# Kernel optimization log

Hardware: AMD Instinct MI355X
Metric: run time of the kernel (lower is better)

The kernel has to match this reference:

```python
import jax, jax.numpy as jnp
import numpy as np


def _l2_normalize(x):
    # matches features.div(features.norm(2, 1, keepdim=True))
    return x / jnp.linalg.norm(x, ord=2, axis=1, keepdims=True)


def setup_inputs() -> dict:
    key = jax.random.key(0)
    k1, k2, k3 = jax.random.split(key, 3)
    B, N, D, C = 2048, 100000, 512, 1000
    return {
        "features": jax.random.normal(k1, (B, D), dtype=jnp.float32),
        "logits": jax.random.normal(k2, (B, C), dtype=jnp.float32),
        "db_features": jax.random.normal(k3, (N, D), dtype=jnp.float32),
        "k": 10,
    }


def reference(features, logits, db_features, k):
    # fit(): index.add(normalize(db_features)) -- faiss IndexFlatL2 stores rows
    xb = _l2_normalize(db_features)            # [N, D]
    # forward(): search normalized queries, take k-th (largest of the k) squared L2 dist
    xq = _l2_normalize(features)               # [B, D]
    # squared L2 distances via the expansion ||q||^2 + ||x||^2 - 2 q.x (faiss IndexFlatL2
    # returns SQUARED distances)
    q2 = jnp.sum(xq * xq, axis=1, keepdims=True)           # [B, 1]
    x2 = jnp.sum(xb * xb, axis=1)                          # [N]
    d2 = q2 + x2[None, :] - 2.0 * (xq @ xb.T)              # [B, N]
    # k smallest distances == k largest of -d2
    neg_topk, _ = jax.lax.top_k(-d2, k)                    # [B, k], sorted descending
    kth = -neg_topk[:, -1]                                 # k-th nearest squared distance
    return kth.reshape(-1, 1)
```

## Files before the change

### kernel.cpp

```cpp
#include <hip/hip_runtime.h>
#include <hip/hip_bf16.h>

typedef unsigned short ushort_t;
typedef unsigned char uchar_t;
typedef __attribute__((ext_vector_type(4))) int int4v;
typedef __attribute__((ext_vector_type(2))) unsigned int uint2v;

#define NQ      2048
#define ND      512
#define NDB     100000
#define TOPK    10
#define NCHUNK  98
#define CHUNK_N 1024
#define NPAD    (NCHUNK * CHUNK_N)
#define QTILES  (NQ / 128)
#define NTILES  (CHUNK_N / 128)
#define NWG     (NCHUNK * QTILES)
#define PERXCD  (NWG / 8)
#define QSCALE  400.0f
#define QINV    (1.0f / (QSCALE * QSCALE))
#define IMIN    (-2147483647 - 1)

#define GL2LDS(gp, lp) __builtin_amdgcn_global_load_lds(                      \
    (const __attribute__((address_space(1))) void*)(gp),                     \
    (__attribute__((address_space(3))) void*)(lp), 16, 0, 0)

__global__ void normalize_rows_i8(const float* __restrict__ in, uchar_t* __restrict__ out,
                                  int nvalid, int ntotal) {
    int row  = blockIdx.x * 4 + (threadIdx.x >> 6);
    int lane = threadIdx.x & 63;
    if (row >= ntotal) return;
    uint2v pk;
    if (row >= nvalid) {
        pk[0] = 0u; pk[1] = 0u;
    } else {
        const float4* src = reinterpret_cast<const float4*>(in + (size_t)row * ND);
        float4 v0 = src[lane * 2];
        float4 v1 = src[lane * 2 + 1];
        float s = v0.x*v0.x + v0.y*v0.y + v0.z*v0.z + v0.w*v0.w
                + v1.x*v1.x + v1.y*v1.y + v1.z*v1.z + v1.w*v1.w;
        #pragma unroll
        for (int off = 32; off; off >>= 1) s += __shfl_xor(s, off, 64);
        float r = rsqrtf(s) * QSCALE;
        float f[8] = { v0.x, v0.y, v0.z, v0.w, v1.x, v1.y, v1.z, v1.w };
        unsigned b[8];
        #pragma unroll
        for (int i = 0; i < 8; ++i) {
            int q = (int)rintf(f[i] * r);
            q = q > 127 ? 127 : (q < -127 ? -127 : q);
            b[i] = (unsigned)q & 0xFFu;
        }
        pk[0] = b[0] | (b[1] << 8) | (b[2] << 16) | (b[3] << 24);
        pk[1] = b[4] | (b[5] << 8) | (b[6] << 16) | (b[7] << 24);
    }
    *reinterpret_cast<uint2v*>(out + (size_t)row * ND + lane * 8) = pk;
}

__device__ inline void topk_insert_i(int (&top)[TOPK], int x) {
    #pragma unroll
    for (int i = 0; i < TOPK; ++i) {
        int mx = top[i] > x ? top[i] : x;
        int mn = top[i] > x ? x : top[i];
        top[i] = mx;
        x = mn;
    }
}

__global__ __launch_bounds__(512, 8)
void knn_chunk(const uchar_t* __restrict__ qb, const uchar_t* __restrict__ dbb,
               int* __restrict__ partial) {
    const int logical = (blockIdx.x & 7) * PERXCD + (blockIdx.x >> 3);
    const int qt = logical & (QTILES - 1);
    const int nc = logical >> 4;
    const int t = threadIdx.x, lane = t & 63, wv = t >> 6;
    const int l15 = lane & 15;

    __shared__ __align__(16) uchar_t As[128 * 64];
    __shared__ __align__(16) uchar_t Bs[128 * 64];

    int top[TOPK];
    #pragma unroll
    for (int i = 0; i < TOPK; ++i) top[i] = IMIN;

    const size_t nchunkbase = (size_t)nc * CHUNK_N;
    const uchar_t* aseg = qb + (size_t)(qt * 128) * ND;

    const int srow = t >> 2;
    const int scol = (t & 3) ^ ((srow >> 1) & 3);
    const int soff = srow * ND + scol * 16;
    const int doff = t * 16;
    const int cgrp = lane >> 4;
    const int slot = (cgrp ^ ((l15 >> 1) & 3)) * 16;
    const int aoff = (wv * 16 + l15) * 64 + slot;
    const int boff = l15 * 64 + slot;

    for (int nt = 0; nt < NTILES; ++nt) {
        const uchar_t* bseg = dbb + (nchunkbase + nt * 128) * ND;
        int4v acc[8];
        #pragma unroll
        for (int b = 0; b < 8; ++b) acc[b] = (int4v){0, 0, 0, 0};

        #pragma unroll
        for (int ks = 0; ks < 8; ++ks) {
            const int kbase = ks * 64;
            __syncthreads();
            GL2LDS(aseg + soff + kbase, As + doff);
            GL2LDS(bseg + soff + kbase, Bs + doff);
            __syncthreads();
            int4v af = *reinterpret_cast<const int4v*>(As + aoff);
            {
                int4v bf0 = *reinterpret_cast<const int4v*>(Bs + boff);
                int4v bf1 = *reinterpret_cast<const int4v*>(Bs + boff + 1024);
                int4v bf2 = *reinterpret_cast<const int4v*>(Bs + boff + 2048);
                int4v bf3 = *reinterpret_cast<const int4v*>(Bs + boff + 3072);
                acc[0] = __builtin_amdgcn_mfma_i32_16x16x64_i8(bf0, af, acc[0], 0, 0, 0);
                acc[1] = __builtin_amdgcn_mfma_i32_16x16x64_i8(bf1, af, acc[1], 0, 0, 0);
                acc[2] = __builtin_amdgcn_mfma_i32_16x16x64_i8(bf2, af, acc[2], 0, 0, 0);
                acc[3] = __builtin_amdgcn_mfma_i32_16x16x64_i8(bf3, af, acc[3], 0, 0, 0);
            }
            {
                int4v bf4 = *reinterpret_cast<const int4v*>(Bs + boff + 4096);
                int4v bf5 = *reinterpret_cast<const int4v*>(Bs + boff + 5120);
                int4v bf6 = *reinterpret_cast<const int4v*>(Bs + boff + 6144);
                int4v bf7 = *reinterpret_cast<const int4v*>(Bs + boff + 7168);
                acc[4] = __builtin_amdgcn_mfma_i32_16x16x64_i8(bf4, af, acc[4], 0, 0, 0);
                acc[5] = __builtin_amdgcn_mfma_i32_16x16x64_i8(bf5, af, acc[5], 0, 0, 0);
                acc[6] = __builtin_amdgcn_mfma_i32_16x16x64_i8(bf6, af, acc[6], 0, 0, 0);
                acc[7] = __builtin_amdgcn_mfma_i32_16x16x64_i8(bf7, af, acc[7], 0, 0, 0);
            }
        }

        int m = acc[0][0];
        #pragma unroll
        for (int ns = 0; ns < 8; ++ns)
            #pragma unroll
            for (int r = 0; r < 4; ++r)
                m = m > acc[ns][r] ? m : acc[ns][r];
        if (m > top[TOPK - 1]) {
            #pragma unroll
            for (int ns = 0; ns < 8; ++ns)
                #pragma unroll
                for (int r = 0; r < 4; ++r) {
                    int v = acc[ns][r];
                    if (v > top[TOPK - 1]) topk_insert_i(top, v);
                }
        }
    }

    #pragma unroll
    for (int step = 16; step <= 32; step <<= 1) {
        int other[TOPK];
        #pragma unroll
        for (int i = 0; i < TOPK; ++i) other[i] = __shfl_xor(top[i], step, 64);
        #pragma unroll
        for (int i = 0; i < TOPK; ++i)
            if (other[i] > top[TOPK - 1]) topk_insert_i(top, other[i]);
    }

    if ((lane >> 4) == 0) {
        const int q = qt * 128 + wv * 16 + l15;
        int* dst = partial + ((size_t)nc * NQ + q) * TOPK;
        #pragma unroll
        for (int i = 0; i < TOPK; ++i) dst[i] = top[i];
    }
}

__global__ void final_merge(const int* __restrict__ partial, float* __restrict__ out) {
    const int q = blockIdx.x * 4 + (threadIdx.x >> 6);
    const int lane = threadIdx.x & 63;
    if (q >= NQ) return;
    int top[TOPK];
    #pragma unroll
    for (int i = 0; i < TOPK; ++i) top[i] = IMIN;
    for (int c = lane; c < NCHUNK; c += 64) {
        const int* p = partial + ((size_t)c * NQ + q) * TOPK;
        #pragma unroll
        for (int i = 0; i < TOPK; ++i) {
            int x = p[i];
            if (x > top[TOPK - 1]) topk_insert_i(top, x);
        }
    }
    #pragma unroll
    for (int step = 1; step <= 32; step <<= 1) {
        int other[TOPK];
        #pragma unroll
        for (int i = 0; i < TOPK; ++i) other[i] = __shfl_xor(top[i], step, 64);
        #pragma unroll
        for (int i = 0; i < TOPK; ++i)
            if (other[i] > top[TOPK - 1]) topk_insert_i(top, other[i]);
    }
    if (lane == 0) out[q] = 2.0f - 2.0f * ((float)top[TOPK - 1] * QINV);
}

extern "C" void kernel_launch(void* const* d_in, const int* in_sizes, int n_in,
                              void* d_out, int out_size, void* d_ws, size_t ws_size,
                              hipStream_t stream) {
    const float* features = (const float*)d_in[0];
    const float* dbf      = (const float*)d_in[2];
    float* out = (float*)d_out;

    uchar_t* dbb = (uchar_t*)d_ws;
    uchar_t* qbn = dbb + (size_t)NPAD * ND;
    int* partial = (int*)(qbn + (size_t)NQ * ND);

    normalize_rows_i8<<<NPAD / 4, 256, 0, stream>>>(dbf, dbb, NDB, NPAD);
    normalize_rows_i8<<<NQ / 4, 256, 0, stream>>>(features, qbn, NQ, NQ);
    knn_chunk<<<NWG, 512, 0, stream>>>(qbn, dbb, partial);
    final_merge<<<NQ / 4, 256, 0, stream>>>(partial, out);
}
```

Measured before the change: 301.6 us.

## Double-buffer LDS tiles to overlap global-to-LDS loads with MFMA

```diff
diff --git a/kernel.cpp b/kernel.cpp
--- a/kernel.cpp
+++ b/kernel.cpp
@@ -75,8 +75,8 @@
     const int t = threadIdx.x, lane = t & 63, wv = t >> 6;
     const int l15 = lane & 15;
 
-    __shared__ __align__(16) uchar_t As[128 * 64];
-    __shared__ __align__(16) uchar_t Bs[128 * 64];
+    __shared__ __align__(16) uchar_t As[2][128 * 64];
+    __shared__ __align__(16) uchar_t Bs[2][128 * 64];
 
     int top[TOPK];
     #pragma unroll
@@ -94,6 +94,12 @@
     const int aoff = (wv * 16 + l15) * 64 + slot;
     const int boff = l15 * 64 + slot;
 
+    {
+        const uchar_t* bseg0 = dbb + nchunkbase * ND;
+        GL2LDS(aseg + soff, As[0] + doff);
+        GL2LDS(bseg0 + soff, Bs[0] + doff);
+    }
+
     for (int nt = 0; nt < NTILES; ++nt) {
         const uchar_t* bseg = dbb + (nchunkbase + nt * 128) * ND;
         int4v acc[8];
@@ -102,27 +108,36 @@
 
         #pragma unroll
         for (int ks = 0; ks < 8; ++ks) {
-            const int kbase = ks * 64;
-            __syncthreads();
-            GL2LDS(aseg + soff + kbase, As + doff);
-            GL2LDS(bseg + soff + kbase, Bs + doff);
-            __syncthreads();
-            int4v af = *reinterpret_cast<const int4v*>(As + aoff);
+            asm volatile("s_waitcnt vmcnt(0)" ::: "memory");
+            __builtin_amdgcn_s_barrier();
+            asm volatile("" ::: "memory");
+
+            if (ks < 7) {
+                GL2LDS(aseg + soff + (ks + 1) * 64, As[(ks + 1) & 1] + doff);
+                GL2LDS(bseg + soff + (ks + 1) * 64, Bs[(ks + 1) & 1] + doff);
+            } else if (nt + 1 < NTILES) {
+                GL2LDS(aseg + soff, As[0] + doff);
+                GL2LDS(bseg + 128 * ND + soff, Bs[0] + doff);
+            }
+
+            const uchar_t* Ac = As[ks & 1];
+            const uchar_t* Bc = Bs[ks & 1];
+            int4v af = *reinterpret_cast<const int4v*>(Ac + aoff);
             {
-                int4v bf0 = *reinterpret_cast<const int4v*>(Bs + boff);
-                int4v bf1 = *reinterpret_cast<const int4v*>(Bs + boff + 1024);
-                int4v bf2 = *reinterpret_cast<const int4v*>(Bs + boff + 2048);
-                int4v bf3 = *reinterpret_cast<const int4v*>(Bs + boff + 3072);
+                int4v bf0 = *reinterpret_cast<const int4v*>(Bc + boff);
+                int4v bf1 = *reinterpret_cast<const int4v*>(Bc + boff + 1024);
+                int4v bf2 = *reinterpret_cast<const int4v*>(Bc + boff + 2048);
+                int4v bf3 = *reinterpret_cast<const int4v*>(Bc + boff + 3072);
                 acc[0] = __builtin_amdgcn_mfma_i32_16x16x64_i8(bf0, af, acc[0], 0, 0, 0);
                 acc[1] = __builtin_amdgcn_mfma_i32_16x16x64_i8(bf1, af, acc[1], 0, 0, 0);
                 acc[2] = __builtin_amdgcn_mfma_i32_16x16x64_i8(bf2, af, acc[2], 0, 0, 0);
                 acc[3] = __builtin_amdgcn_mfma_i32_16x16x64_i8(bf3, af, acc[3], 0, 0, 0);
             }
             {
-                int4v bf4 = *reinterpret_cast<const int4v*>(Bs + boff + 4096);
-                int4v bf5 = *reinterpret_cast<const int4v*>(Bs + boff + 5120);
-                int4v bf6 = *reinterpret_cast<const int4v*>(Bs + boff + 6144);
-                int4v bf7 = *reinterpret_cast<const int4v*>(Bs + boff + 7168);
+                int4v bf4 = *reinterpret_cast<const int4v*>(Bc + boff + 4096);
+                int4v bf5 = *reinterpret_cast<const int4v*>(Bc + boff + 5120);
+                int4v bf6 = *reinterpret_cast<const int4v*>(Bc + boff + 6144);
+                int4v bf7 = *reinterpret_cast<const int4v*>(Bc + boff + 7168);
                 acc[4] = __builtin_amdgcn_mfma_i32_16x16x64_i8(bf4, af, acc[4], 0, 0, 0);
                 acc[5] = __builtin_amdgcn_mfma_i32_16x16x64_i8(bf5, af, acc[5], 0, 0, 0);
                 acc[6] = __builtin_amdgcn_mfma_i32_16x16x64_i8(bf6, af, acc[6], 0, 0, 0);
```

New measurement: 344.7 us. 14.3% more time.

## Retile wave work to 32 queries by 64 db rows per wave

Applied to the files above, without the earlier changes.

```diff
diff --git a/kernel.cpp b/kernel.cpp
--- a/kernel.cpp
+++ b/kernel.cpp
@@ -74,13 +74,16 @@
     const int nc = logical >> 4;
     const int t = threadIdx.x, lane = t & 63, wv = t >> 6;
     const int l15 = lane & 15;
+    const int qg = wv >> 1, nh = wv & 1;
 
     __shared__ __align__(16) uchar_t As[128 * 64];
     __shared__ __align__(16) uchar_t Bs[128 * 64];
 
-    int top[TOPK];
-    #pragma unroll
-    for (int i = 0; i < TOPK; ++i) top[i] = IMIN;
+    int top[2][TOPK];
+    #pragma unroll
+    for (int qs = 0; qs < 2; ++qs)
+        #pragma unroll
+        for (int i = 0; i < TOPK; ++i) top[qs][i] = IMIN;
 
     const size_t nchunkbase = (size_t)nc * CHUNK_N;
     const uchar_t* aseg = qb + (size_t)(qt * 128) * ND;
@@ -91,14 +94,16 @@
     const int doff = t * 16;
     const int cgrp = lane >> 4;
     const int slot = (cgrp ^ ((l15 >> 1) & 3)) * 16;
-    const int aoff = (wv * 16 + l15) * 64 + slot;
-    const int boff = l15 * 64 + slot;
+    const int aoff = (qg * 32 + l15) * 64 + slot;
+    const int boff = (nh * 64 + l15) * 64 + slot;
 
     for (int nt = 0; nt < NTILES; ++nt) {
         const uchar_t* bseg = dbb + (nchunkbase + nt * 128) * ND;
-        int4v acc[8];
-        #pragma unroll
-        for (int b = 0; b < 8; ++b) acc[b] = (int4v){0, 0, 0, 0};
+        int4v acc[2][4];
+        #pragma unroll
+        for (int a = 0; a < 2; ++a)
+            #pragma unroll
+            for (int b = 0; b < 4; ++b) acc[a][b] = (int4v){0, 0, 0, 0};
 
         #pragma unroll
         for (int ks = 0; ks < 8; ++ks) {
@@ -107,61 +112,63 @@
             GL2LDS(aseg + soff + kbase, As + doff);
             GL2LDS(bseg + soff + kbase, Bs + doff);
             __syncthreads();
-            int4v af = *reinterpret_cast<const int4v*>(As + aoff);
-            {
-                int4v bf0 = *reinterpret_cast<const int4v*>(Bs + boff);
-                int4v bf1 = *reinterpret_cast<const int4v*>(Bs + boff + 1024);
-                int4v bf2 = *reinterpret_cast<const int4v*>(Bs + boff + 2048);
-                int4v bf3 = *reinterpret_cast<const int4v*>(Bs + boff + 3072);
-                acc[0] = __builtin_amdgcn_mfma_i32_16x16x64_i8(bf0, af, acc[0], 0, 0, 0);
-                acc[1] = __builtin_amdgcn_mfma_i32_16x16x64_i8(bf1, af, acc[1], 0, 0, 0);
-                acc[2] = __builtin_amdgcn_mfma_i32_16x16x64_i8(bf2, af, acc[2], 0, 0, 0);
-                acc[3] = __builtin_amdgcn_mfma_i32_16x16x64_i8(bf3, af, acc[3], 0, 0, 0);
+            int4v af0 = *reinterpret_cast<const int4v*>(As + aoff);
+            int4v af1 = *reinterpret_cast<const int4v*>(As + aoff + 1024);
+            int4v bf0 = *reinterpret_cast<const int4v*>(Bs + boff);
+            int4v bf1 = *reinterpret_cast<const int4v*>(Bs + boff + 1024);
+            int4v bf2 = *reinterpret_cast<const int4v*>(Bs + boff + 2048);
+            int4v bf3 = *reinterpret_cast<const int4v*>(Bs + boff + 3072);
+            acc[0][0] = __builtin_amdgcn_mfma_i32_16x16x64_i8(bf0, af0, acc[0][0], 0, 0, 0);
+            acc[0][1] = __builtin_amdgcn_mfma_i32_16x16x64_i8(bf1, af0, acc[0][1], 0, 0, 0);
+            acc[0][2] = __builtin_amdgcn_mfma_i32_16x16x64_i8(bf2, af0, acc[0][2], 0, 0, 0);
+            acc[0][3] = __builtin_amdgcn_mfma_i32_16x16x64_i8(bf3, af0, acc[0][3], 0, 0, 0);
+            acc[1][0] = __builtin_amdgcn_mfma_i32_16x16x64_i8(bf0, af1, acc[1][0], 0, 0, 0);
+            acc[1][1] = __builtin_amdgcn_mfma_i32_16x16x64_i8(bf1, af1, acc[1][1], 0, 0, 0);
+            acc[1][2] = __builtin_amdgcn_mfma_i32_16x16x64_i8(bf2, af1, acc[1][2], 0, 0, 0);
+            acc[1][3] = __builtin_amdgcn_mfma_i32_16x16x64_i8(bf3, af1, acc[1][3], 0, 0, 0);
+        }
+
+        #pragma unroll
+        for (int qs = 0; qs < 2; ++qs) {
+            int m = acc[qs][0][0];
+            #pragma unroll
+            for (int ns = 0; ns < 4; ++ns)
+                #pragma unroll
+                for (int r = 0; r < 4; ++r)
+                    m = m > acc[qs][ns][r] ? m : acc[qs][ns][r];
+            if (m > top[qs][TOPK - 1]) {
+                #pragma unroll
+                for (int ns = 0; ns < 4; ++ns)
+                    #pragma unroll
+                    for (int r = 0; r < 4; ++r) {
+                        int v = acc[qs][ns][r];
+                        if (v > top[qs][TOPK - 1]) topk_insert_i(top[qs], v);
+                    }
             }
-            {
-                int4v bf4 = *reinterpret_cast<const int4v*>(Bs + boff + 4096);
-                int4v bf5 = *reinterpret_cast<const int4v*>(Bs + boff + 5120);
-                int4v bf6 = *reinterpret_cast<const int4v*>(Bs + boff + 6144);
-                int4v bf7 = *reinterpret_cast<const int4v*>(Bs + boff + 7168);
-                acc[4] = __builtin_amdgcn_mfma_i32_16x16x64_i8(bf4, af, acc[4], 0, 0, 0);
-                acc[5] = __builtin_amdgcn_mfma_i32_16x16x64_i8(bf5, af, acc[5], 0, 0, 0);
-                acc[6] = __builtin_amdgcn_mfma_i32_16x16x64_i8(bf6, af, acc[6], 0, 0, 0);
-                acc[7] = __builtin_amdgcn_mfma_i32_16x16x64_i8(bf7, af, acc[7], 0, 0, 0);
-            }
-        }
-
-        int m = acc[0][0];
-        #pragma unroll
-        for (int ns = 0; ns < 8; ++ns)
-            #pragma unroll
-            for (int r = 0; r < 4; ++r)
-                m = m > acc[ns][r] ? m : acc[ns][r];
-        if (m > top[TOPK - 1]) {
-            #pragma unroll
-            for (int ns = 0; ns < 8; ++ns)
-                #pragma unroll
-                for (int r = 0; r < 4; ++r) {
-                    int v = acc[ns][r];
-                    if (v > top[TOPK - 1]) topk_insert_i(top, v);
-                }
-        }
-    }
-
-    #pragma unroll
-    for (int step = 16; step <= 32; step <<= 1) {
-        int other[TOPK];
-        #pragma unroll
-        for (int i = 0; i < TOPK; ++i) other[i] = __shfl_xor(top[i], step, 64);
-        #pragma unroll
-        for (int i = 0; i < TOPK; ++i)
-            if (other[i] > top[TOPK - 1]) topk_insert_i(top, other[i]);
+        }
+    }
+
+    #pragma unroll
+    for (int qs = 0; qs < 2; ++qs) {
+        #pragma unroll
+        for (int step = 16; step <= 32; step <<= 1) {
+            int other[TOPK];
+            #pragma unroll
+            for (int i = 0; i < TOPK; ++i) other[i] = __shfl_xor(top[qs][i], step, 64);
+            #pragma unroll
+            for (int i = 0; i < TOPK; ++i)
+                if (other[i] > top[qs][TOPK - 1]) topk_insert_i(top[qs], other[i]);
+        }
     }
 
     if ((lane >> 4) == 0) {
-        const int q = qt * 128 + wv * 16 + l15;
-        int* dst = partial + ((size_t)nc * NQ + q) * TOPK;
-        #pragma unroll
-        for (int i = 0; i < TOPK; ++i) dst[i] = top[i];
+        #pragma unroll
+        for (int qs = 0; qs < 2; ++qs) {
+            const int q = qt * 128 + qg * 32 + qs * 16 + l15;
+            int* dst = partial + (((size_t)(nc * 2 + nh)) * NQ + q) * TOPK;
+            #pragma unroll
+            for (int i = 0; i < TOPK; ++i) dst[i] = top[qs][i];
+        }
     }
 }
 
@@ -172,7 +179,7 @@
     int top[TOPK];
     #pragma unroll
     for (int i = 0; i < TOPK; ++i) top[i] = IMIN;
-    for (int c = lane; c < NCHUNK; c += 64) {
+    for (int c = lane; c < 2 * NCHUNK; c += 64) {
         const int* p = partial + ((size_t)c * NQ + q) * TOPK;
         #pragma unroll
         for (int i = 0; i < TOPK; ++i) {
```

New measurement: 401.9 us. 33.3% more time.
